# Kernel optimization log

Measured on AMD Instinct MI355X. Metric: run time of the kernel, lower is better.

The kernel has to match this reference:

```python
import jax, jax.numpy as jnp
import numpy as np

NUM_GROUPS = 8
EPS = 1e-5


def group_norm(x, gamma, beta):
    # x: [B, C, H, W], groups over channel dim
    b, c, h, w = x.shape
    xg = x.reshape(b, NUM_GROUPS, c // NUM_GROUPS, h, w)
    mean = xg.mean(axis=(2, 3, 4), keepdims=True)
    var = xg.var(axis=(2, 3, 4), keepdims=True)
    xg = (xg - mean) * jax.lax.rsqrt(var + EPS)
    x = xg.reshape(b, c, h, w)
    return x * gamma[None, :, None, None] + beta[None, :, None, None]


def conv1x1(x, w, bias):
    # 1x1 conv == per-pixel linear: [B,C,H,W] x [O,C] -> [B,O,H,W]
    return jnp.einsum('bchw,oc->bohw', x, w) + bias[None, :, None, None]


def setup_inputs() -> dict:
    key = jax.random.key(0)
    ks = jax.random.split(key, 6)
    B, C, H, W = 16, 512, 32, 32
    s = 1.0 / np.sqrt(C)  # conv2d default init scale-ish
    return {
        'x': jax.random.normal(ks[0], (B, C, H, W), jnp.float32),
        'gn_w': jnp.ones((C,), jnp.float32),
        'gn_b': jnp.zeros((C,), jnp.float32),
        'wq': jax.random.normal(ks[1], (C, C), jnp.float32) * s,
        'bq': jnp.zeros((C,), jnp.float32),
        'wk': jax.random.normal(ks[2], (C, C), jnp.float32) * s,
        'bk': jnp.zeros((C,), jnp.float32),
        'wv': jax.random.normal(ks[3], (C, C), jnp.float32) * s,
        'bv': jnp.zeros((C,), jnp.float32),
        'wo': jax.random.normal(ks[4], (C, C), jnp.float32) * s,
        'bo': jnp.zeros((C,), jnp.float32),
    }


def reference(x, gn_w, gn_b, wq, bq, wk, bk, wv, bv, wo, bo):
    b, c, h, w = x.shape
    scale = c ** (-0.5)
    hn = group_norm(x, gn_w, gn_b)
    q = conv1x1(hn, wq, bq).reshape(b, c, h * w).transpose(0, 2, 1)  # [B, N, C]
    k = conv1x1(hn, wk, bk).reshape(b, c, h * w).transpose(0, 2, 1)  # [B, N, C]
    v = conv1x1(hn, wv, bv).reshape(b, c, h * w).transpose(0, 2, 1)  # [B, N, C]
    attn = jnp.einsum('bnc,bmc->bnm', q, k) * scale                 # [B, N, N]
    attn = jax.nn.softmax(attn, axis=-1)
    out = jnp.einsum('bnm,bmc->bnc', attn, v)                       # [B, N, C]
    out = out.transpose(0, 2, 1).reshape(b, c, h, w)
    out = conv1x1(out, wo, bo)
    return x + out
```

## Files before the change

kernel.cpp:

```cpp
#include <hip/hip_runtime.h>
#include <stdint.h>

#define C_DIM 512
#define HW_N  1024
#define CPG   64
#define EPS_GN 1e-5f
#define SCALE_QK 0.044194173824159216f

typedef __attribute__((ext_vector_type(8))) __bf16 bf16x8v;
typedef __attribute__((ext_vector_type(4))) float  f32x4;

typedef __attribute__((address_space(1))) void gvoid_t;
typedef __attribute__((address_space(3))) void lvoid_t;

constexpr long long SNC = (long long)HW_N * C_DIM;
constexpr long long SNN = (long long)HW_N * 1024;

__device__ __forceinline__ void gload_lds16(const void* g, void* l) {
  __builtin_amdgcn_global_load_lds((gvoid_t*)g, (lvoid_t*)l, 16, 0, 0);
}

__device__ __forceinline__ uint16_t f2bfbits(float f) {
  __bf16 h = (__bf16)f;
  return __builtin_bit_cast(uint16_t, h);
}

__device__ __forceinline__ float bf2f(uint16_t u) {
  return __builtin_bit_cast(float, (uint32_t)u << 16);
}

template<int N>
__device__ __forceinline__ void vm_wait() {
  if constexpr (N == 0)      asm volatile("s_waitcnt vmcnt(0)" ::: "memory");
  else if constexpr (N == 2) asm volatile("s_waitcnt vmcnt(2)" ::: "memory");
  else if constexpr (N == 3) asm volatile("s_waitcnt vmcnt(3)" ::: "memory");
  else                       asm volatile("s_waitcnt vmcnt(6)" ::: "memory");
}

struct BlkId { int bx, by, bz; };
__device__ __forceinline__ BlkId xcd_decode(int gx, int gy) {
  const int nwg = gridDim.x;
  const int bid = blockIdx.x;
  const int wg  = (bid & 7) * (nwg >> 3) + (bid >> 3);
  const int pb  = gx * gy;
  const int bz  = wg / pb;
  const int rem = wg - bz * pb;
  const int by  = rem / gx;
  const int bx  = rem - by * gx;
  return {bx, by, bz};
}

__global__ __launch_bounds__(256)
void prep_stats_kernel(const float* __restrict__ wq, const float* __restrict__ wk,
                       const float* __restrict__ wv, const float* __restrict__ wo,
                       const float* __restrict__ bq, const float* __restrict__ bk,
                       const float* __restrict__ x,
                       __bf16* __restrict__ wqkb, __bf16* __restrict__ wvb,
                       __bf16* __restrict__ wob, float* __restrict__ bqk,
                       float2* __restrict__ part)
{
  const int blk = blockIdx.x;
  const int t = threadIdx.x;
  if (blk < 1024) {
    const int which = blk >> 8;
    const int i = (blk & 255) * 256 + t;
    const float* src = (which == 0) ? wq : (which == 1) ? wk : (which == 2) ? wv : wo;
    __bf16* dst = (which == 0) ? wqkb
               : (which == 1) ? (wqkb + (size_t)C_DIM * C_DIM)
               : (which == 2) ? wvb : wob;
    const float scale = (which == 0) ? SCALE_QK : 1.f;
    float4 v = ((const float4*)src)[i];
    uint32_t lo = (uint32_t)f2bfbits(v.x * scale) | ((uint32_t)f2bfbits(v.y * scale) << 16);
    uint32_t hi = (uint32_t)f2bfbits(v.z * scale) | ((uint32_t)f2bfbits(v.w * scale) << 16);
    ((uint2*)dst)[i] = make_uint2(lo, hi);
  } else if (blk == 1024) {
    for (int j = t; j < 1024; j += 256)
      bqk[j] = (j < 512) ? bq[j] * SCALE_QK : bk[j - 512];
  } else {
    const int lin  = blk - 1025;
    const int b    = lin >> 4;
    const int g    = (lin >> 1) & 7;
    const int half = lin & 1;
    const float4* xv = (const float4*)(x + ((long long)(b * C_DIM + g * CPG)) * HW_N
                                         + half * 512);
    float s1 = 0.f, s2 = 0.f;
    for (int i = t; i < 64 * 128; i += 256) {
      const int c  = i >> 7;
      const int nf = i & 127;
      float4 v = xv[c * 256 + nf];
      s1 += v.x + v.y + v.z + v.w;
      s2 += v.x * v.x + v.y * v.y + v.z * v.z + v.w * v.w;
    }
    #pragma unroll
    for (int off = 32; off; off >>= 1) {
      s1 += __shfl_xor(s1, off);
      s2 += __shfl_xor(s2, off);
    }
    __shared__ float red[2][4];
    const int w = t >> 6, l = t & 63;
    if (l == 0) { red[0][w] = s1; red[1][w] = s2; }
    __syncthreads();
    if (t == 0) {
      s1 = red[0][0] + red[0][1] + red[0][2] + red[0][3];
      s2 = red[1][0] + red[1][1] + red[1][2] + red[1][3];
      part[lin] = make_float2(s1, s2);
    }
  }
}

__global__ __launch_bounds__(512)
void gn_norm(const float* __restrict__ x, const float2* __restrict__ part,
             const float* __restrict__ gnw, const float* __restrict__ gnb,
             __bf16* __restrict__ hn)
{
  const int b  = blockIdx.x >> 4;
  const int nc = blockIdx.x & 15;
  const int t  = threadIdx.x;

  __shared__ float asc[512], bsc[512];
  __shared__ float tile[64][65];

  {
    const int c = t;
    const int g = c >> 6;
    float2 p0 = part[(b * 8 + g) * 2 + 0];
    float2 p1 = part[(b * 8 + g) * 2 + 1];
    const float mean = (p0.x + p1.x) * (1.f / 65536.f);
    const float var  = (p0.y + p1.y) * (1.f / 65536.f) - mean * mean;
    const float rstd = rsqrtf(var + EPS_GN);
    const float a = rstd * gnw[c];
    asc[c] = a;
    bsc[c] = gnb[c] - mean * a;
  }
  __syncthreads();

  const long long xb = (long long)b * C_DIM * HW_N + nc * 64;
  __bf16* ob = hn + ((long long)b * HW_N + nc * 64) * C_DIM;

  for (int cg = 0; cg < 8; ++cg) {
    #pragma unroll
    for (int pass = 0; pass < 2; ++pass) {
      const int task = pass * 512 + t;
      const int c  = task >> 4;
      const int f4 = task & 15;
      float4 v = *(const float4*)(x + xb + (long long)(cg * 64 + c) * HW_N + f4 * 4);
      const float a  = asc[cg * 64 + c];
      const float bb = bsc[cg * 64 + c];
      tile[c][f4 * 4 + 0] = v.x * a + bb;
      tile[c][f4 * 4 + 1] = v.y * a + bb;
      tile[c][f4 * 4 + 2] = v.z * a + bb;
      tile[c][f4 * 4 + 3] = v.w * a + bb;
    }
    __syncthreads();
    {
      const int n  = t >> 3;
      const int gc = t & 7;
      uint32_t p[4];
      #pragma unroll
      for (int j = 0; j < 4; ++j) {
        const float f0 = tile[gc * 8 + 2 * j + 0][n];
        const float f1 = tile[gc * 8 + 2 * j + 1][n];
        p[j] = (uint32_t)f2bfbits(f0) | ((uint32_t)f2bfbits(f1) << 16);
      }
      *(uint4*)(ob + (long long)n * C_DIM + cg * 64 + gc * 8) =
          make_uint4(p[0], p[1], p[2], p[3]);
    }
    __syncthreads();
  }
}

__global__ __launch_bounds__(256)
void softmax_kernel(__bf16* __restrict__ S)
{
  const long long row = blockIdx.x;
  uint2* sp = (uint2*)(S + row * HW_N);
  const int t = threadIdx.x;
  uint2 raw = sp[t];
  float v0 = bf2f((uint16_t)(raw.x & 0xffff));
  float v1 = bf2f((uint16_t)(raw.x >> 16));
  float v2 = bf2f((uint16_t)(raw.y & 0xffff));
  float v3 = bf2f((uint16_t)(raw.y >> 16));
  float m = fmaxf(fmaxf(v0, v1), fmaxf(v2, v3));
  #pragma unroll
  for (int off = 32; off; off >>= 1) m = fmaxf(m, __shfl_xor(m, off));
  __shared__ float redm[4];
  __shared__ float reds[4];
  const int w = t >> 6, l = t & 63;
  if (l == 0) redm[w] = m;
  __syncthreads();
  m = fmaxf(fmaxf(redm[0], redm[1]), fmaxf(redm[2], redm[3]));
  float e0 = __expf(v0 - m), e1 = __expf(v1 - m);
  float e2 = __expf(v2 - m), e3 = __expf(v3 - m);
  float sum = e0 + e1 + e2 + e3;
  #pragma unroll
  for (int off = 32; off; off >>= 1) sum += __shfl_xor(sum, off);
  if (l == 0) reds[w] = sum;
  __syncthreads();
  sum = reds[0] + reds[1] + reds[2] + reds[3];
  const float inv = 1.f / sum;
  uint32_t lo = (uint32_t)f2bfbits(e0 * inv) | ((uint32_t)f2bfbits(e1 * inv) << 16);
  uint32_t hi = (uint32_t)f2bfbits(e2 * inv) | ((uint32_t)f2bfbits(e3 * inv) << 16);
  sp[t] = make_uint2(lo, hi);
}

template<int BN, int OUTM, int BIASM>
__device__ __forceinline__ void gemm_body(char* lds,
    const __bf16* __restrict__ Ab, const __bf16* __restrict__ Bb,
    void* __restrict__ Cb, const float* __restrict__ bias,
    const float* __restrict__ resid,
    int lda, int ldb, int ldc, int K, int m0, int n0)
{
  constexpr int CB = BN / 128;
  constexpr int CH = 1 + CB;
  constexpr int NF = BN / 64;
  constexpr int TILE_B = 8192 * CH;

  const int tt = threadIdx.x;
  const int w  = tt >> 6;
  const int l  = tt & 63;
  const int lr = l & 15;
  const int lg = l >> 4;
  const int wm = w >> 2;
  const int wn = w & 3;

  const int srow = tt >> 2;
  const int sgr  = (tt & 3) ^ ((tt >> 3) & 3);

  f32x4 acc[4][NF];
  #pragma unroll
  for (int f = 0; f < 4; ++f)
    #pragma unroll
    for (int c = 0; c < NF; ++c)
      acc[f][c] = (f32x4){0.f, 0.f, 0.f, 0.f};

  auto stage = [&](int t, int c) {
    char* dst = lds + (t % 3) * TILE_B + c * 8192 + w * 1024;
    const __bf16* src = (c == 0)
      ? Ab + (long long)(m0 + srow) * lda + (t << 5) + sgr * 8
      : Bb + (long long)(n0 + (c - 1) * 128 + srow) * ldb + (t << 5) + sgr * 8;
    gload_lds16(src, dst);
  };
  auto rdA = [&](const char* base, int f) -> bf16x8v {
    const int row = wm * 64 + f * 16 + lr;
    return *(const bf16x8v*)(base + row * 64 + ((lg ^ ((row >> 1) & 3)) << 4));
  };
  auto rdB = [&](const char* base, int c) -> bf16x8v {
    const int row = wn * (BN / 4) + c * 16 + lr;
    return *(const bf16x8v*)(base + 8192 + row * 64 + ((lg ^ ((row >> 1) & 3)) << 4));
  };

  const int NT = K >> 5;

  #pragma unroll
  for (int c = 0; c < CH; ++c) stage(0, c);
  #pragma unroll
  for (int c = 0; c < CH; ++c) stage(1, c);
  vm_wait<CH>();
  __builtin_amdgcn_s_barrier();
  __builtin_amdgcn_sched_barrier(0);

  for (int t = 0; t < NT; ++t) {
    const char* buf = lds + (t % 3) * TILE_B;

    if (t + 2 < NT) {
      #pragma unroll
      for (int c = 0; c < CH; ++c) stage(t + 2, c);
    }
    bf16x8v Bf[NF], Af[4];
    #pragma unroll
    for (int c = 0; c < NF; ++c) Bf[c] = rdB(buf, c);
    #pragma unroll
    for (int f = 0; f < 4; ++f)  Af[f] = rdA(buf, f);
    #pragma unroll
    for (int f = 0; f < 4; ++f)
      #pragma unroll
      for (int c = 0; c < NF; ++c)
        acc[f][c] = __builtin_amdgcn_mfma_f32_16x16x32_bf16(Af[f], Bf[c], acc[f][c], 0, 0, 0);
    __builtin_amdgcn_sched_barrier(0);
    if (t + 2 < NT) vm_wait<CH>();
    else            vm_wait<0>();
    __builtin_amdgcn_s_barrier();
    __builtin_amdgcn_sched_barrier(0);
  }

  #pragma unroll
  for (int f = 0; f < 4; ++f) {
    const int rrb = m0 + wm * 64 + f * 16 + lg * 4;
    #pragma unroll
    for (int c = 0; c < NF; ++c) {
      const int cc = n0 + wn * (BN / 4) + c * 16 + lr;
      const float cbias = (BIASM == 1) ? bias[cc] : 0.f;
      #pragma unroll
      for (int r = 0; r < 4; ++r) {
        const int rr = rrb + r;
        float v = acc[f][c][r];
        if (BIASM == 1) v += cbias;
        if (BIASM == 2) v += bias[rr];
        const long long idx = (long long)rr * ldc + cc;
        if (OUTM == 0) {
          ((__bf16*)Cb)[idx] = (__bf16)v;
        } else if (OUTM == 2) {
          ((float*)Cb)[idx] = v;
        } else {
          ((float*)Cb)[idx] = v + resid[idx];
        }
      }
    }
  }
}

__global__ __launch_bounds__(512, 4)
void qkv_kernel(const __bf16* __restrict__ hn, const __bf16* __restrict__ wqkb,
                const __bf16* __restrict__ wvb,
                __bf16* __restrict__ qkb, __bf16* __restrict__ vtb,
                const float* __restrict__ bqk, const float* __restrict__ bv)
{
  __shared__ alignas(16) char lds[73728];
  const int wg = (blockIdx.x & 7) * 96 + (blockIdx.x >> 3);
  if (wg < 512) {
    const int bz = wg >> 5, rem = wg & 31, by = rem >> 2, bx = rem & 3;
    gemm_body<256, 0, 1>(lds, hn + (long long)bz * SNC, wqkb,
                         (void*)(qkb + (long long)bz * SNN), bqk, nullptr,
                         C_DIM, C_DIM, 1024, C_DIM, by * 128, bx * 256);
  } else {
    const int wg2 = wg - 512;
    const int bz = wg2 >> 4, rem = wg2 & 15, by = rem >> 2, bx = rem & 3;
    gemm_body<256, 0, 2>(lds, wvb, hn + (long long)bz * SNC,
                         (void*)(vtb + (long long)bz * SNC), bv, nullptr,
                         C_DIM, C_DIM, HW_N, C_DIM, by * 128, bx * 256);
  }
}

template<int BN, int OUTM, int BIASM>
__global__ __launch_bounds__(512, 4)
void gemm8k(const __bf16* __restrict__ A, const __bf16* __restrict__ B,
            void* __restrict__ C, const float* __restrict__ bias,
            const float* __restrict__ resid,
            int lda, int ldb, int ldc,
            long long aS, long long bS, long long cS, int K, int gx, int gy)
{
  __shared__ alignas(16) char lds[8192 * (1 + BN / 128) * 3];
  const BlkId id = xcd_decode(gx, gy);
  const __bf16* Ab = A + (long long)id.bz * aS;
  const __bf16* Bb = B + (long long)id.bz * bS;
  void* Cb = (OUTM == 0) ? (void*)((__bf16*)C + (long long)id.bz * cS)
                         : (void*)((float*)C + (long long)id.bz * cS);
  const float* rb = (OUTM == 1) ? (resid + (long long)id.bz * cS) : nullptr;
  gemm_body<BN, OUTM, BIASM>(lds, Ab, Bb, Cb, bias, rb,
                             lda, ldb, ldc, K, id.by * 128, id.bx * BN);
}

extern "C" void kernel_launch(void* const* d_in, const int* in_sizes, int n_in,
                              void* d_out, int out_size, void* d_ws, size_t ws_size,
                              hipStream_t stream)
{
  const float* x   = (const float*)d_in[0];
  const float* gnw = (const float*)d_in[1];
  const float* gnb = (const float*)d_in[2];
  const float* wq  = (const float*)d_in[3];
  const float* bq  = (const float*)d_in[4];
  const float* wk  = (const float*)d_in[5];
  const float* bk  = (const float*)d_in[6];
  const float* wv  = (const float*)d_in[7];
  const float* bv  = (const float*)d_in[8];
  const float* wo  = (const float*)d_in[9];
  const float* bo  = (const float*)d_in[10];
  (void)in_sizes; (void)n_in; (void)out_size; (void)ws_size;

  size_t used = 0;
  char* base = (char*)d_ws;
  auto carve = [&](size_t bytes) -> void* {
    used = (used + 255) & ~(size_t)255;
    void* p = base + used;
    used += bytes;
    return p;
  };

  __bf16* wqkb = (__bf16*)carve((size_t)2 * C_DIM * C_DIM * 2);
  __bf16* wvb  = (__bf16*)carve((size_t)C_DIM * C_DIM * 2);
  __bf16* wob  = (__bf16*)carve((size_t)C_DIM * C_DIM * 2);
  float*  bqk  = (float*) carve((size_t)1024 * 4);
  float2* part = (float2*)carve((size_t)256 * 8);

  __bf16* hn   = (__bf16*)carve((size_t)16 * HW_N * C_DIM * 2);
  __bf16* qkb  = (__bf16*)carve((size_t)16 * HW_N * 1024 * 2);
  __bf16* vtb  = (__bf16*)carve((size_t)16 * C_DIM * HW_N * 2);
  __bf16* o1b  = (__bf16*)carve((size_t)16 * HW_N * C_DIM * 2);
  __bf16* Sb   = (__bf16*)carve((size_t)16 * HW_N * HW_N * 2);

  prep_stats_kernel<<<dim3(1281), 256, 0, stream>>>(wq, wk, wv, wo, bq, bk, x,
                                                    wqkb, wvb, wob, bqk, part);
  gn_norm<<<dim3(256), 512, 0, stream>>>(x, part, gnw, gnb, hn);

  qkv_kernel<<<dim3(768), 512, 0, stream>>>(hn, wqkb, wvb, qkb, vtb, bqk, bv);

  gemm8k<256, 0, 0><<<dim3(512), 512, 0, stream>>>(qkb, qkb + 512, Sb,
      nullptr, nullptr, 1024, 1024, 1024, SNN, SNN, SNN, C_DIM, 4, 8);

  softmax_kernel<<<dim3(16 * 1024), 256, 0, stream>>>(Sb);

  gemm8k<128, 0, 0><<<dim3(512), 512, 0, stream>>>(Sb, vtb, o1b,
      nullptr, nullptr, 1024, 1024, C_DIM, SNN, SNC, SNC, HW_N, 4, 8);

  gemm8k<128, 1, 2><<<dim3(512), 512, 0, stream>>>(wob, o1b, (void*)d_out,
      bo, x, C_DIM, C_DIM, HW_N, 0, SNC, SNC, C_DIM, 8, 4);
}
```

Baseline: 139.2 us.

## Switch GEMMs to wider-N tiles with four-stage LDS pipeline

Replaces the shared GEMM body with a variant whose output tiles are always 256 wide in N and 128 or 256 tall in M. It also deepens the global-to-LDS prefetch ring from three to four stages, with matching vmcnt waits. All GEMM launches get larger tiles and half as many workgroups, and occupancy drops to two blocks per CU. The aim is more data reuse per tile and better hiding of memory latency, at the cost of fewer waves to fill the GPU and more register and LDS pressure.

```diff
diff --git a/kernel.cpp b/kernel.cpp
--- a/kernel.cpp
+++ b/kernel.cpp
@@ -32,9 +32,10 @@
 template<int N>
 __device__ __forceinline__ void vm_wait() {
   if constexpr (N == 0)      asm volatile("s_waitcnt vmcnt(0)" ::: "memory");
-  else if constexpr (N == 2) asm volatile("s_waitcnt vmcnt(2)" ::: "memory");
   else if constexpr (N == 3) asm volatile("s_waitcnt vmcnt(3)" ::: "memory");
-  else                       asm volatile("s_waitcnt vmcnt(6)" ::: "memory");
+  else if constexpr (N == 4) asm volatile("s_waitcnt vmcnt(4)" ::: "memory");
+  else if constexpr (N == 6) asm volatile("s_waitcnt vmcnt(6)" ::: "memory");
+  else if constexpr (N == 8) asm volatile("s_waitcnt vmcnt(8)" ::: "memory");
 }
 
 struct BlkId { int bx, by, bz; };
@@ -203,17 +204,17 @@
   sp[t] = make_uint2(lo, hi);
 }
 
-template<int BN, int OUTM, int BIASM>
-__device__ __forceinline__ void gemm_body(char* lds,
+template<int BM, int OUTM, int BIASM>
+__device__ __forceinline__ void gemm_deep(char* lds,
     const __bf16* __restrict__ Ab, const __bf16* __restrict__ Bb,
     void* __restrict__ Cb, const float* __restrict__ bias,
     const float* __restrict__ resid,
     int lda, int ldb, int ldc, int K, int m0, int n0)
 {
-  constexpr int CB = BN / 128;
-  constexpr int CH = 1 + CB;
-  constexpr int NF = BN / 64;
-  constexpr int TILE_B = 8192 * CH;
+  constexpr int CA   = BM / 128;
+  constexpr int CH   = CA + 2;
+  constexpr int SLOT = BM * 64 + 16384;
+  constexpr int RF   = BM / 32;
 
   const int tt = threadIdx.x;
   const int w  = tt >> 6;
@@ -226,27 +227,27 @@
   const int srow = tt >> 2;
   const int sgr  = (tt & 3) ^ ((tt >> 3) & 3);
 
-  f32x4 acc[4][NF];
-  #pragma unroll
-  for (int f = 0; f < 4; ++f)
-    #pragma unroll
-    for (int c = 0; c < NF; ++c)
+  f32x4 acc[RF][4];
+  #pragma unroll
+  for (int f = 0; f < RF; ++f)
+    #pragma unroll
+    for (int c = 0; c < 4; ++c)
       acc[f][c] = (f32x4){0.f, 0.f, 0.f, 0.f};
 
   auto stage = [&](int t, int c) {
-    char* dst = lds + (t % 3) * TILE_B + c * 8192 + w * 1024;
-    const __bf16* src = (c == 0)
-      ? Ab + (long long)(m0 + srow) * lda + (t << 5) + sgr * 8
-      : Bb + (long long)(n0 + (c - 1) * 128 + srow) * ldb + (t << 5) + sgr * 8;
+    char* dst = lds + (t & 3) * SLOT + c * 8192 + w * 1024;
+    const __bf16* src = (c < CA)
+      ? Ab + (long long)(m0 + c * 128 + srow) * lda + (t << 5) + sgr * 8
+      : Bb + (long long)(n0 + (c - CA) * 128 + srow) * ldb + (t << 5) + sgr * 8;
     gload_lds16(src, dst);
   };
   auto rdA = [&](const char* base, int f) -> bf16x8v {
-    const int row = wm * 64 + f * 16 + lr;
+    const int row = wm * (BM / 2) + f * 16 + lr;
     return *(const bf16x8v*)(base + row * 64 + ((lg ^ ((row >> 1) & 3)) << 4));
   };
   auto rdB = [&](const char* base, int c) -> bf16x8v {
-    const int row = wn * (BN / 4) + c * 16 + lr;
-    return *(const bf16x8v*)(base + 8192 + row * 64 + ((lg ^ ((row >> 1) & 3)) << 4));
+    const int row = wn * 64 + c * 16 + lr;
+    return *(const bf16x8v*)(base + BM * 64 + row * 64 + ((lg ^ ((row >> 1) & 3)) << 4));
   };
 
   const int NT = K >> 5;
@@ -255,40 +256,43 @@
   for (int c = 0; c < CH; ++c) stage(0, c);
   #pragma unroll
   for (int c = 0; c < CH; ++c) stage(1, c);
-  vm_wait<CH>();
+  #pragma unroll
+  for (int c = 0; c < CH; ++c) stage(2, c);
+  vm_wait<2 * CH>();
   __builtin_amdgcn_s_barrier();
   __builtin_amdgcn_sched_barrier(0);
 
   for (int t = 0; t < NT; ++t) {
-    const char* buf = lds + (t % 3) * TILE_B;
-
-    if (t + 2 < NT) {
+    const char* buf = lds + (t & 3) * SLOT;
+
+    if (t + 3 < NT) {
       #pragma unroll
-      for (int c = 0; c < CH; ++c) stage(t + 2, c);
-    }
-    bf16x8v Bf[NF], Af[4];
-    #pragma unroll
-    for (int c = 0; c < NF; ++c) Bf[c] = rdB(buf, c);
-    #pragma unroll
-    for (int f = 0; f < 4; ++f)  Af[f] = rdA(buf, f);
-    #pragma unroll
-    for (int f = 0; f < 4; ++f)
+      for (int c = 0; c < CH; ++c) stage(t + 3, c);
+    }
+    bf16x8v Bf[4], Af[RF];
+    #pragma unroll
+    for (int c = 0; c < 4; ++c)  Bf[c] = rdB(buf, c);
+    #pragma unroll
+    for (int f = 0; f < RF; ++f) Af[f] = rdA(buf, f);
+    #pragma unroll
+    for (int f = 0; f < RF; ++f)
       #pragma unroll
-      for (int c = 0; c < NF; ++c)
+      for (int c = 0; c < 4; ++c)
         acc[f][c] = __builtin_amdgcn_mfma_f32_16x16x32_bf16(Af[f], Bf[c], acc[f][c], 0, 0, 0);
     __builtin_amdgcn_sched_barrier(0);
-    if (t + 2 < NT) vm_wait<CH>();
-    else            vm_wait<0>();
+    if (t + 3 < NT)      vm_wait<2 * CH>();
+    else if (t + 2 < NT) vm_wait<CH>();
+    else                 vm_wait<0>();
     __builtin_amdgcn_s_barrier();
     __builtin_amdgcn_sched_barrier(0);
   }
 
   #pragma unroll
-  for (int f = 0; f < 4; ++f) {
-    const int rrb = m0 + wm * 64 + f * 16 + lg * 4;
-    #pragma unroll
-    for (int c = 0; c < NF; ++c) {
-      const int cc = n0 + wn * (BN / 4) + c * 16 + lr;
+  for (int f = 0; f < RF; ++f) {
+    const int rrb = m0 + wm * (BM / 2) + f * 16 + lg * 4;
+    #pragma unroll
+    for (int c = 0; c < 4; ++c) {
+      const int cc = n0 + wn * 64 + c * 16 + lr;
       const float cbias = (BIASM == 1) ? bias[cc] : 0.f;
       #pragma unroll
       for (int r = 0; r < 4; ++r) {
@@ -299,8 +303,6 @@
         const long long idx = (long long)rr * ldc + cc;
         if (OUTM == 0) {
           ((__bf16*)Cb)[idx] = (__bf16)v;
-        } else if (OUTM == 2) {
-          ((float*)Cb)[idx] = v;
         } else {
           ((float*)Cb)[idx] = v + resid[idx];
         }
@@ -309,45 +311,48 @@
   }
 }
 
-__global__ __launch_bounds__(512, 4)
-void qkv_kernel(const __bf16* __restrict__ hn, const __bf16* __restrict__ wqkb,
-                const __bf16* __restrict__ wvb,
-                __bf16* __restrict__ qkb, __bf16* __restrict__ vtb,
-                const float* __restrict__ bqk, const float* __restrict__ bv)
-{
-  __shared__ alignas(16) char lds[73728];
-  const int wg = (blockIdx.x & 7) * 96 + (blockIdx.x >> 3);
-  if (wg < 512) {
-    const int bz = wg >> 5, rem = wg & 31, by = rem >> 2, bx = rem & 3;
-    gemm_body<256, 0, 1>(lds, hn + (long long)bz * SNC, wqkb,
+__global__ __launch_bounds__(512, 2)
+void qkv_deep(const __bf16* __restrict__ hn, const __bf16* __restrict__ wqkb,
+              const __bf16* __restrict__ wvb,
+              __bf16* __restrict__ qkb, __bf16* __restrict__ vtb,
+              const float* __restrict__ bqk, const float* __restrict__ bv)
+{
+  __shared__ alignas(16) char lds[4 * (256 * 64 + 16384)];
+  const int bid  = blockIdx.x;
+  const int half = bid >> 8;
+  const int b8   = bid & 255;
+  const int wg   = (b8 & 7) * 32 + (b8 >> 3);
+  const int bz   = wg >> 4;
+  const int by   = (wg >> 2) & 3;
+  const int bx   = wg & 3;
+  if (half == 0) {
+    gemm_deep<256, 0, 1>(lds, hn + (long long)bz * SNC, wqkb,
                          (void*)(qkb + (long long)bz * SNN), bqk, nullptr,
-                         C_DIM, C_DIM, 1024, C_DIM, by * 128, bx * 256);
+                         C_DIM, C_DIM, 1024, C_DIM, by * 256, bx * 256);
   } else {
-    const int wg2 = wg - 512;
-    const int bz = wg2 >> 4, rem = wg2 & 15, by = rem >> 2, bx = rem & 3;
-    gemm_body<256, 0, 2>(lds, wvb, hn + (long long)bz * SNC,
+    gemm_deep<128, 0, 2>(lds, wvb, hn + (long long)bz * SNC,
                          (void*)(vtb + (long long)bz * SNC), bv, nullptr,
                          C_DIM, C_DIM, HW_N, C_DIM, by * 128, bx * 256);
   }
 }
 
-template<int BN, int OUTM, int BIASM>
-__global__ __launch_bounds__(512, 4)
-void gemm8k(const __bf16* __restrict__ A, const __bf16* __restrict__ B,
-            void* __restrict__ C, const float* __restrict__ bias,
-            const float* __restrict__ resid,
-            int lda, int ldb, int ldc,
-            long long aS, long long bS, long long cS, int K, int gx, int gy)
-{
-  __shared__ alignas(16) char lds[8192 * (1 + BN / 128) * 3];
+template<int BM, int OUTM, int BIASM>
+__global__ __launch_bounds__(512, 2)
+void gdeep(const __bf16* __restrict__ A, const __bf16* __restrict__ B,
+           void* __restrict__ C, const float* __restrict__ bias,
+           const float* __restrict__ resid,
+           int lda, int ldb, int ldc,
+           long long aS, long long bS, long long cS, int K, int gx, int gy)
+{
+  __shared__ alignas(16) char lds[4 * (BM * 64 + 16384)];
   const BlkId id = xcd_decode(gx, gy);
   const __bf16* Ab = A + (long long)id.bz * aS;
   const __bf16* Bb = B + (long long)id.bz * bS;
   void* Cb = (OUTM == 0) ? (void*)((__bf16*)C + (long long)id.bz * cS)
                          : (void*)((float*)C + (long long)id.bz * cS);
   const float* rb = (OUTM == 1) ? (resid + (long long)id.bz * cS) : nullptr;
-  gemm_body<BN, OUTM, BIASM>(lds, Ab, Bb, Cb, bias, rb,
-                             lda, ldb, ldc, K, id.by * 128, id.bx * BN);
+  gemm_deep<BM, OUTM, BIASM>(lds, Ab, Bb, Cb, bias, rb,
+                             lda, ldb, ldc, K, id.by * BM, id.bx * 256);
 }
 
 extern "C" void kernel_launch(void* const* d_in, const int* in_sizes, int n_in,
@@ -392,16 +397,16 @@
                                                     wqkb, wvb, wob, bqk, part);
   gn_norm<<<dim3(256), 512, 0, stream>>>(x, part, gnw, gnb, hn);
 
-  qkv_kernel<<<dim3(768), 512, 0, stream>>>(hn, wqkb, wvb, qkb, vtb, bqk, bv);
-
-  gemm8k<256, 0, 0><<<dim3(512), 512, 0, stream>>>(qkb, qkb + 512, Sb,
-      nullptr, nullptr, 1024, 1024, 1024, SNN, SNN, SNN, C_DIM, 4, 8);
+  qkv_deep<<<dim3(512), 512, 0, stream>>>(hn, wqkb, wvb, qkb, vtb, bqk, bv);
+
+  gdeep<256, 0, 0><<<dim3(256), 512, 0, stream>>>(qkb, qkb + 512, Sb,
+      nullptr, nullptr, 1024, 1024, 1024, SNN, SNN, SNN, C_DIM, 4, 4);
 
   softmax_kernel<<<dim3(16 * 1024), 256, 0, stream>>>(Sb);
 
-  gemm8k<128, 0, 0><<<dim3(512), 512, 0, stream>>>(Sb, vtb, o1b,
-      nullptr, nullptr, 1024, 1024, C_DIM, SNN, SNC, SNC, HW_N, 4, 8);
-
-  gemm8k<128, 1, 2><<<dim3(512), 512, 0, stream>>>(wob, o1b, (void*)d_out,
-      bo, x, C_DIM, C_DIM, HW_N, 0, SNC, SNC, C_DIM, 8, 4);
-}
+  gdeep<128, 0, 0><<<dim3(256), 512, 0, stream>>>(Sb, vtb, o1b,
+      nullptr, nullptr, 1024, 1024, C_DIM, SNN, SNC, SNC, HW_N, 2, 8);
+
+  gdeep<128, 1, 2><<<dim3(256), 512, 0, stream>>>(wob, o1b, (void*)d_out,
+      bo, x, C_DIM, C_DIM, HW_N, 0, SNC, SNC, C_DIM, 4, 4);
+}
```

Result: no change. 139.1 us (-0.1%).

## Use 256x256 output tiles for QKV and QK^T GEMMs

Applied to the files above, without the earlier changes.

Adds a new GEMM body with 256x256 output tiles per 512-thread block, where each wave computes 64x128, and uses it for the QKV projection and the Q·K^T score GEMM. Each block moves from 128x256 tiles to 256x256, halving the number of blocks. The aim is more reuse of each staged operand tile and less global and LDS traffic per FLOP. The cost is larger LDS use (96KB, three-stage buffers), about 128 accumulator registers per thread and lower occupancy (launch bounds 2). The smaller grids (384 and 256 blocks) may also leave compute units underused.

```diff
diff --git a/kernel.cpp b/kernel.cpp
--- a/kernel.cpp
+++ b/kernel.cpp
@@ -31,10 +31,16 @@
 
 template<int N>
 __device__ __forceinline__ void vm_wait() {
-  if constexpr (N == 0)      asm volatile("s_waitcnt vmcnt(0)" ::: "memory");
-  else if constexpr (N == 2) asm volatile("s_waitcnt vmcnt(2)" ::: "memory");
-  else if constexpr (N == 3) asm volatile("s_waitcnt vmcnt(3)" ::: "memory");
-  else                       asm volatile("s_waitcnt vmcnt(6)" ::: "memory");
+  static_assert(N >= 0 && N <= 8, "vm_wait: unsupported count");
+  if constexpr (N == 0) asm volatile("s_waitcnt vmcnt(0)" ::: "memory");
+  if constexpr (N == 1) asm volatile("s_waitcnt vmcnt(1)" ::: "memory");
+  if constexpr (N == 2) asm volatile("s_waitcnt vmcnt(2)" ::: "memory");
+  if constexpr (N == 3) asm volatile("s_waitcnt vmcnt(3)" ::: "memory");
+  if constexpr (N == 4) asm volatile("s_waitcnt vmcnt(4)" ::: "memory");
+  if constexpr (N == 5) asm volatile("s_waitcnt vmcnt(5)" ::: "memory");
+  if constexpr (N == 6) asm volatile("s_waitcnt vmcnt(6)" ::: "memory");
+  if constexpr (N == 7) asm volatile("s_waitcnt vmcnt(7)" ::: "memory");
+  if constexpr (N == 8) asm volatile("s_waitcnt vmcnt(8)" ::: "memory");
 }
 
 struct BlkId { int bx, by, bz; };
@@ -203,6 +209,108 @@
   sp[t] = make_uint2(lo, hi);
 }
 
+template<int OUTM, int BIASM>
+__device__ __forceinline__ void gemm_fat(char* lds,
+    const __bf16* __restrict__ Ab, const __bf16* __restrict__ Bb,
+    void* __restrict__ Cb, const float* __restrict__ bias,
+    const float* __restrict__ resid,
+    int lda, int ldb, int ldc, int K, int m0, int n0)
+{
+  constexpr int SLOT = 32768;
+  constexpr int CH   = 4;
+
+  const int tt = threadIdx.x;
+  const int w  = tt >> 6;
+  const int l  = tt & 63;
+  const int lr = l & 15;
+  const int lg = l >> 4;
+  const int wm = w >> 1;
+  const int wn = w & 1;
+
+  const int srow = tt >> 2;
+  const int sgr  = (tt & 3) ^ ((tt >> 3) & 3);
+
+  f32x4 acc[4][8];
+  #pragma unroll
+  for (int f = 0; f < 4; ++f)
+    #pragma unroll
+    for (int c = 0; c < 8; ++c)
+      acc[f][c] = (f32x4){0.f, 0.f, 0.f, 0.f};
+
+  auto stage = [&](int t, int c) {
+    char* dst = lds + (t % 3) * SLOT + c * 8192 + w * 1024;
+    const __bf16* src = (c < 2)
+      ? Ab + (long long)(m0 + c * 128 + srow) * lda + (t << 5) + sgr * 8
+      : Bb + (long long)(n0 + (c - 2) * 128 + srow) * ldb + (t << 5) + sgr * 8;
+    gload_lds16(src, dst);
+  };
+  auto rdA = [&](const char* base, int f) -> bf16x8v {
+    const int row = wm * 64 + f * 16 + lr;
+    return *(const bf16x8v*)(base + row * 64 + ((lg ^ ((row >> 1) & 3)) << 4));
+  };
+  auto rdB = [&](const char* base, int c) -> bf16x8v {
+    const int row = wn * 128 + c * 16 + lr;
+    return *(const bf16x8v*)(base + 16384 + row * 64 + ((lg ^ ((row >> 1) & 3)) << 4));
+  };
+
+  const int NT = K >> 5;
+
+  #pragma unroll
+  for (int c = 0; c < CH; ++c) stage(0, c);
+  #pragma unroll
+  for (int c = 0; c < CH; ++c) stage(1, c);
+  vm_wait<CH>();
+  __builtin_amdgcn_s_barrier();
+  __builtin_amdgcn_sched_barrier(0);
+
+  for (int t = 0; t < NT; ++t) {
+    const char* buf = lds + (t % 3) * SLOT;
+
+    if (t + 2 < NT) {
+      #pragma unroll
+      for (int c = 0; c < CH; ++c) stage(t + 2, c);
+    }
+    bf16x8v Bf[8], Af[4];
+    #pragma unroll
+    for (int c = 0; c < 8; ++c) Bf[c] = rdB(buf, c);
+    #pragma unroll
+    for (int f = 0; f < 4; ++f) Af[f] = rdA(buf, f);
+    #pragma unroll
+    for (int f = 0; f < 4; ++f)
+      #pragma unroll
+      for (int c = 0; c < 8; ++c)
+        acc[f][c] = __builtin_amdgcn_mfma_f32_16x16x32_bf16(Af[f], Bf[c], acc[f][c], 0, 0, 0);
+    __builtin_amdgcn_sched_barrier(0);
+    if (t + 2 < NT) vm_wait<CH>();
+    else            vm_wait<0>();
+    __builtin_amdgcn_s_barrier();
+    __builtin_amdgcn_sched_barrier(0);
+  }
+
+  #pragma unroll
+  for (int f = 0; f < 4; ++f) {
+    const int rrb = m0 + wm * 64 + f * 16 + lg * 4;
+    #pragma unroll
+    for (int c = 0; c < 8; ++c) {
+      const int cc = n0 + wn * 128 + c * 16 + lr;
+      const float cbias = (BIASM == 1) ? bias[cc] : 0.f;
+      #pragma unroll
+      for (int r = 0; r < 4; ++r) {
+        const int rr = rrb + r;
+        float v = acc[f][c][r];
+        if (BIASM == 1) v += cbias;
+        if (BIASM == 2) v += bias[rr];
+        const long long idx = (long long)rr * ldc + cc;
+        if (OUTM == 0) {
+          ((__bf16*)Cb)[idx] = (__bf16)v;
+        } else {
+          ((float*)Cb)[idx] = v + resid[idx];
+        }
+      }
+    }
+  }
+}
+
 template<int BN, int OUTM, int BIASM>
 __device__ __forceinline__ void gemm_body(char* lds,
     const __bf16* __restrict__ Ab, const __bf16* __restrict__ Bb,
@@ -309,26 +417,38 @@
   }
 }
 
-__global__ __launch_bounds__(512, 4)
-void qkv_kernel(const __bf16* __restrict__ hn, const __bf16* __restrict__ wqkb,
-                const __bf16* __restrict__ wvb,
-                __bf16* __restrict__ qkb, __bf16* __restrict__ vtb,
-                const float* __restrict__ bqk, const float* __restrict__ bv)
-{
-  __shared__ alignas(16) char lds[73728];
-  const int wg = (blockIdx.x & 7) * 96 + (blockIdx.x >> 3);
-  if (wg < 512) {
-    const int bz = wg >> 5, rem = wg & 31, by = rem >> 2, bx = rem & 3;
-    gemm_body<256, 0, 1>(lds, hn + (long long)bz * SNC, wqkb,
-                         (void*)(qkb + (long long)bz * SNN), bqk, nullptr,
-                         C_DIM, C_DIM, 1024, C_DIM, by * 128, bx * 256);
+__global__ __launch_bounds__(512, 2)
+void qkv_fat(const __bf16* __restrict__ hn, const __bf16* __restrict__ wqkb,
+             const __bf16* __restrict__ wvb,
+             __bf16* __restrict__ qkb, __bf16* __restrict__ vtb,
+             const float* __restrict__ bqk, const float* __restrict__ bv)
+{
+  __shared__ alignas(16) char lds[98304];
+  const int bid = blockIdx.x;
+  const int wg  = (bid & 7) * 48 + (bid >> 3);
+  if (wg < 256) {
+    const int bz = wg >> 4, rem = wg & 15, by = rem >> 2, bx = rem & 3;
+    gemm_fat<0, 1>(lds, hn + (long long)bz * SNC, wqkb,
+                   (void*)(qkb + (long long)bz * SNN), bqk, nullptr,
+                   C_DIM, C_DIM, 1024, C_DIM, by * 256, bx * 256);
   } else {
-    const int wg2 = wg - 512;
-    const int bz = wg2 >> 4, rem = wg2 & 15, by = rem >> 2, bx = rem & 3;
-    gemm_body<256, 0, 2>(lds, wvb, hn + (long long)bz * SNC,
-                         (void*)(vtb + (long long)bz * SNC), bv, nullptr,
-                         C_DIM, C_DIM, HW_N, C_DIM, by * 128, bx * 256);
-  }
+    const int wg2 = wg - 256;
+    const int bz = wg2 >> 3, rem = wg2 & 7, by = rem >> 2, bx = rem & 3;
+    gemm_fat<0, 2>(lds, wvb, hn + (long long)bz * SNC,
+                   (void*)(vtb + (long long)bz * SNC), bv, nullptr,
+                   C_DIM, C_DIM, HW_N, C_DIM, by * 256, bx * 256);
+  }
+}
+
+__global__ __launch_bounds__(512, 2)
+void s_fat(const __bf16* __restrict__ qkb, __bf16* __restrict__ Sb)
+{
+  __shared__ alignas(16) char lds[98304];
+  const BlkId id = xcd_decode(4, 4);
+  gemm_fat<0, 0>(lds, qkb + (long long)id.bz * SNN,
+                 qkb + (long long)id.bz * SNN + 512,
+                 (void*)(Sb + (long long)id.bz * SNN), nullptr, nullptr,
+                 1024, 1024, 1024, C_DIM, id.by * 256, id.bx * 256);
 }
 
 template<int BN, int OUTM, int BIASM>
@@ -392,10 +512,9 @@
                                                     wqkb, wvb, wob, bqk, part);
   gn_norm<<<dim3(256), 512, 0, stream>>>(x, part, gnw, gnb, hn);
 
-  qkv_kernel<<<dim3(768), 512, 0, stream>>>(hn, wqkb, wvb, qkb, vtb, bqk, bv);
-
-  gemm8k<256, 0, 0><<<dim3(512), 512, 0, stream>>>(qkb, qkb + 512, Sb,
-      nullptr, nullptr, 1024, 1024, 1024, SNN, SNN, SNN, C_DIM, 4, 8);
+  qkv_fat<<<dim3(384), 512, 0, stream>>>(hn, wqkb, wvb, qkb, vtb, bqk, bv);
+
+  s_fat<<<dim3(256), 512, 0, stream>>>(qkb, Sb);
 
   softmax_kernel<<<dim3(16 * 1024), 256, 0, stream>>>(Sb);
 
```

Measured after the change: 140.0 us. Within noise of the previous version (+0.5%).

## Deepen GEMM K-step to 64 and unify all GEMMs on 128x256 tiles

Applied to the files above, without the earlier changes.

Replaces the templated GEMM body with a single 128x256 tile kernel that stages 64-wide K slices per pipeline step with a new 8-way XOR swizzle, doubling MFMA work per barrier. The PV and output-projection GEMMs move from 128x128 tiles (512 blocks) to 128x256 tiles (256 blocks). LDS per block rises to 144 KB with occupancy hint lowered to 2, so fewer waves hide latency and the smaller grids may underfill the 256 CUs.

```diff
diff --git a/kernel.cpp b/kernel.cpp
--- a/kernel.cpp
+++ b/kernel.cpp
@@ -31,10 +31,17 @@
 
 template<int N>
 __device__ __forceinline__ void vm_wait() {
-  if constexpr (N == 0)      asm volatile("s_waitcnt vmcnt(0)" ::: "memory");
-  else if constexpr (N == 2) asm volatile("s_waitcnt vmcnt(2)" ::: "memory");
-  else if constexpr (N == 3) asm volatile("s_waitcnt vmcnt(3)" ::: "memory");
-  else                       asm volatile("s_waitcnt vmcnt(6)" ::: "memory");
+  static_assert(N >= 0 && N <= 12, "vm_wait: unsupported count");
+  if constexpr (N == 0)  asm volatile("s_waitcnt vmcnt(0)"  ::: "memory");
+  if constexpr (N == 1)  asm volatile("s_waitcnt vmcnt(1)"  ::: "memory");
+  if constexpr (N == 2)  asm volatile("s_waitcnt vmcnt(2)"  ::: "memory");
+  if constexpr (N == 3)  asm volatile("s_waitcnt vmcnt(3)"  ::: "memory");
+  if constexpr (N == 4)  asm volatile("s_waitcnt vmcnt(4)"  ::: "memory");
+  if constexpr (N == 5)  asm volatile("s_waitcnt vmcnt(5)"  ::: "memory");
+  if constexpr (N == 6)  asm volatile("s_waitcnt vmcnt(6)"  ::: "memory");
+  if constexpr (N == 7)  asm volatile("s_waitcnt vmcnt(7)"  ::: "memory");
+  if constexpr (N == 8)  asm volatile("s_waitcnt vmcnt(8)"  ::: "memory");
+  if constexpr (N == 12) asm volatile("s_waitcnt vmcnt(12)" ::: "memory");
 }
 
 struct BlkId { int bx, by, bz; };
@@ -203,17 +210,15 @@
   sp[t] = make_uint2(lo, hi);
 }
 
-template<int BN, int OUTM, int BIASM>
-__device__ __forceinline__ void gemm_body(char* lds,
+template<int OUTM, int BIASM>
+__device__ __forceinline__ void gemm64(char* lds,
     const __bf16* __restrict__ Ab, const __bf16* __restrict__ Bb,
     void* __restrict__ Cb, const float* __restrict__ bias,
     const float* __restrict__ resid,
     int lda, int ldb, int ldc, int K, int m0, int n0)
 {
-  constexpr int CB = BN / 128;
-  constexpr int CH = 1 + CB;
-  constexpr int NF = BN / 64;
-  constexpr int TILE_B = 8192 * CH;
+  constexpr int SLOT = 49152;
+  constexpr int CH   = 6;
 
   const int tt = threadIdx.x;
   const int w  = tt >> 6;
@@ -223,33 +228,33 @@
   const int wm = w >> 2;
   const int wn = w & 3;
 
-  const int srow = tt >> 2;
-  const int sgr  = (tt & 3) ^ ((tt >> 3) & 3);
-
-  f32x4 acc[4][NF];
+  const int srow = tt >> 3;
+  const int sg   = (tt & 7) ^ (srow & 7);
+
+  f32x4 acc[4][4];
   #pragma unroll
   for (int f = 0; f < 4; ++f)
     #pragma unroll
-    for (int c = 0; c < NF; ++c)
+    for (int c = 0; c < 4; ++c)
       acc[f][c] = (f32x4){0.f, 0.f, 0.f, 0.f};
 
   auto stage = [&](int t, int c) {
-    char* dst = lds + (t % 3) * TILE_B + c * 8192 + w * 1024;
-    const __bf16* src = (c == 0)
-      ? Ab + (long long)(m0 + srow) * lda + (t << 5) + sgr * 8
-      : Bb + (long long)(n0 + (c - 1) * 128 + srow) * ldb + (t << 5) + sgr * 8;
+    char* dst = lds + (t % 3) * SLOT + c * 8192 + w * 1024;
+    const __bf16* src = (c < 2)
+      ? Ab + (long long)(m0 + c * 64 + srow) * lda + (t << 6) + sg * 8
+      : Bb + (long long)(n0 + (c - 2) * 64 + srow) * ldb + (t << 6) + sg * 8;
     gload_lds16(src, dst);
   };
-  auto rdA = [&](const char* base, int f) -> bf16x8v {
+  auto rdA = [&](const char* base, int f, int kk) -> bf16x8v {
     const int row = wm * 64 + f * 16 + lr;
-    return *(const bf16x8v*)(base + row * 64 + ((lg ^ ((row >> 1) & 3)) << 4));
+    return *(const bf16x8v*)(base + row * 128 + ((((kk << 2) + lg) ^ (row & 7)) << 4));
   };
-  auto rdB = [&](const char* base, int c) -> bf16x8v {
-    const int row = wn * (BN / 4) + c * 16 + lr;
-    return *(const bf16x8v*)(base + 8192 + row * 64 + ((lg ^ ((row >> 1) & 3)) << 4));
+  auto rdB = [&](const char* base, int c, int kk) -> bf16x8v {
+    const int row = wn * 64 + c * 16 + lr;
+    return *(const bf16x8v*)(base + 16384 + row * 128 + ((((kk << 2) + lg) ^ (row & 7)) << 4));
   };
 
-  const int NT = K >> 5;
+  const int NT = K >> 6;
 
   #pragma unroll
   for (int c = 0; c < CH; ++c) stage(0, c);
@@ -260,22 +265,29 @@
   __builtin_amdgcn_sched_barrier(0);
 
   for (int t = 0; t < NT; ++t) {
-    const char* buf = lds + (t % 3) * TILE_B;
+    const char* buf = lds + (t % 3) * SLOT;
 
     if (t + 2 < NT) {
       #pragma unroll
       for (int c = 0; c < CH; ++c) stage(t + 2, c);
     }
-    bf16x8v Bf[NF], Af[4];
-    #pragma unroll
-    for (int c = 0; c < NF; ++c) Bf[c] = rdB(buf, c);
-    #pragma unroll
-    for (int f = 0; f < 4; ++f)  Af[f] = rdA(buf, f);
+    bf16x8v Af[4][2], Bf[4][2];
+    #pragma unroll
+    for (int c = 0; c < 4; ++c)
+      #pragma unroll
+      for (int kk = 0; kk < 2; ++kk) Bf[c][kk] = rdB(buf, c, kk);
     #pragma unroll
     for (int f = 0; f < 4; ++f)
       #pragma unroll
-      for (int c = 0; c < NF; ++c)
-        acc[f][c] = __builtin_amdgcn_mfma_f32_16x16x32_bf16(Af[f], Bf[c], acc[f][c], 0, 0, 0);
+      for (int kk = 0; kk < 2; ++kk) Af[f][kk] = rdA(buf, f, kk);
+    #pragma unroll
+    for (int f = 0; f < 4; ++f)
+      #pragma unroll
+      for (int c = 0; c < 4; ++c)
+        #pragma unroll
+        for (int kk = 0; kk < 2; ++kk)
+          acc[f][c] = __builtin_amdgcn_mfma_f32_16x16x32_bf16(Af[f][kk], Bf[c][kk],
+                                                              acc[f][c], 0, 0, 0);
     __builtin_amdgcn_sched_barrier(0);
     if (t + 2 < NT) vm_wait<CH>();
     else            vm_wait<0>();
@@ -287,8 +299,8 @@
   for (int f = 0; f < 4; ++f) {
     const int rrb = m0 + wm * 64 + f * 16 + lg * 4;
     #pragma unroll
-    for (int c = 0; c < NF; ++c) {
-      const int cc = n0 + wn * (BN / 4) + c * 16 + lr;
+    for (int c = 0; c < 4; ++c) {
+      const int cc = n0 + wn * 64 + c * 16 + lr;
       const float cbias = (BIASM == 1) ? bias[cc] : 0.f;
       #pragma unroll
       for (int r = 0; r < 4; ++r) {
@@ -309,45 +321,45 @@
   }
 }
 
-__global__ __launch_bounds__(512, 4)
+__global__ __launch_bounds__(512, 2)
 void qkv_kernel(const __bf16* __restrict__ hn, const __bf16* __restrict__ wqkb,
                 const __bf16* __restrict__ wvb,
                 __bf16* __restrict__ qkb, __bf16* __restrict__ vtb,
                 const float* __restrict__ bqk, const float* __restrict__ bv)
 {
-  __shared__ alignas(16) char lds[73728];
+  __shared__ alignas(16) char lds[147456];
   const int wg = (blockIdx.x & 7) * 96 + (blockIdx.x >> 3);
   if (wg < 512) {
     const int bz = wg >> 5, rem = wg & 31, by = rem >> 2, bx = rem & 3;
-    gemm_body<256, 0, 1>(lds, hn + (long long)bz * SNC, wqkb,
-                         (void*)(qkb + (long long)bz * SNN), bqk, nullptr,
-                         C_DIM, C_DIM, 1024, C_DIM, by * 128, bx * 256);
+    gemm64<0, 1>(lds, hn + (long long)bz * SNC, wqkb,
+                 (void*)(qkb + (long long)bz * SNN), bqk, nullptr,
+                 C_DIM, C_DIM, 1024, C_DIM, by * 128, bx * 256);
   } else {
     const int wg2 = wg - 512;
     const int bz = wg2 >> 4, rem = wg2 & 15, by = rem >> 2, bx = rem & 3;
-    gemm_body<256, 0, 2>(lds, wvb, hn + (long long)bz * SNC,
-                         (void*)(vtb + (long long)bz * SNC), bv, nullptr,
-                         C_DIM, C_DIM, HW_N, C_DIM, by * 128, bx * 256);
-  }
-}
-
-template<int BN, int OUTM, int BIASM>
-__global__ __launch_bounds__(512, 4)
-void gemm8k(const __bf16* __restrict__ A, const __bf16* __restrict__ B,
-            void* __restrict__ C, const float* __restrict__ bias,
-            const float* __restrict__ resid,
-            int lda, int ldb, int ldc,
-            long long aS, long long bS, long long cS, int K, int gx, int gy)
-{
-  __shared__ alignas(16) char lds[8192 * (1 + BN / 128) * 3];
+    gemm64<0, 2>(lds, wvb, hn + (long long)bz * SNC,
+                 (void*)(vtb + (long long)bz * SNC), bv, nullptr,
+                 C_DIM, C_DIM, HW_N, C_DIM, by * 128, bx * 256);
+  }
+}
+
+template<int OUTM, int BIASM>
+__global__ __launch_bounds__(512, 2)
+void gemm64k(const __bf16* __restrict__ A, const __bf16* __restrict__ B,
+             void* __restrict__ C, const float* __restrict__ bias,
+             const float* __restrict__ resid,
+             int lda, int ldb, int ldc,
+             long long aS, long long bS, long long cS, int K, int gx, int gy)
+{
+  __shared__ alignas(16) char lds[147456];
   const BlkId id = xcd_decode(gx, gy);
   const __bf16* Ab = A + (long long)id.bz * aS;
   const __bf16* Bb = B + (long long)id.bz * bS;
   void* Cb = (OUTM == 0) ? (void*)((__bf16*)C + (long long)id.bz * cS)
                          : (void*)((float*)C + (long long)id.bz * cS);
   const float* rb = (OUTM == 1) ? (resid + (long long)id.bz * cS) : nullptr;
-  gemm_body<BN, OUTM, BIASM>(lds, Ab, Bb, Cb, bias, rb,
-                             lda, ldb, ldc, K, id.by * 128, id.bx * BN);
+  gemm64<OUTM, BIASM>(lds, Ab, Bb, Cb, bias, rb,
+                      lda, ldb, ldc, K, id.by * 128, id.bx * 256);
 }
 
 extern "C" void kernel_launch(void* const* d_in, const int* in_sizes, int n_in,
@@ -394,14 +406,14 @@
 
   qkv_kernel<<<dim3(768), 512, 0, stream>>>(hn, wqkb, wvb, qkb, vtb, bqk, bv);
 
-  gemm8k<256, 0, 0><<<dim3(512), 512, 0, stream>>>(qkb, qkb + 512, Sb,
+  gemm64k<0, 0><<<dim3(512), 512, 0, stream>>>(qkb, qkb + 512, Sb,
       nullptr, nullptr, 1024, 1024, 1024, SNN, SNN, SNN, C_DIM, 4, 8);
 
   softmax_kernel<<<dim3(16 * 1024), 256, 0, stream>>>(Sb);
 
-  gemm8k<128, 0, 0><<<dim3(512), 512, 0, stream>>>(Sb, vtb, o1b,
-      nullptr, nullptr, 1024, 1024, C_DIM, SNN, SNC, SNC, HW_N, 4, 8);
-
-  gemm8k<128, 1, 2><<<dim3(512), 512, 0, stream>>>(wob, o1b, (void*)d_out,
-      bo, x, C_DIM, C_DIM, HW_N, 0, SNC, SNC, C_DIM, 8, 4);
-}
+  gemm64k<0, 0><<<dim3(256), 512, 0, stream>>>(Sb, vtb, o1b,
+      nullptr, nullptr, 1024, 1024, C_DIM, SNN, SNC, SNC, HW_N, 2, 8);
+
+  gemm64k<1, 2><<<dim3(256), 512, 0, stream>>>(wob, o1b, (void*)d_out,
+      bo, x, C_DIM, C_DIM, HW_N, 0, SNC, SNC, C_DIM, 4, 4);
+}
```

New measurement: 140.3 us. No clear change (+0.8%).
